# Optimization experiments

Measured on AMD Instinct MI355X. Metric: run time of the kernel, lower is better.

The kernel has to match this reference:

```python
import jax, jax.numpy as jnp
import numpy as np

N = 100000
IN_C = 128
OUT_C = 128
E = 1600000


def setup_inputs() -> dict:
    key = jax.random.key(0)
    k1, k2, k3, k4 = jax.random.split(key, 4)
    x = jax.random.normal(k1, (N, IN_C), dtype=jnp.float32)
    edge_index = jax.random.randint(k2, (2, E), 0, N, dtype=jnp.int64)
    # GCNConv params: linear weight (stored [in, out] for x @ W) and bias [out]
    W = jax.random.normal(k3, (IN_C, OUT_C), dtype=jnp.float32) / np.sqrt(IN_C)
    b = jax.random.normal(k4, (OUT_C,), dtype=jnp.float32) * 0.01
    return {"x": x, "edge_index": edge_index, "W": W, "b": b}


def reference(x, edge_index, W, b):
    n = x.shape[0]
    # add self loops (PyG GCNConv default add_self_loops=True)
    loop = jnp.arange(n, dtype=edge_index.dtype)
    src = jnp.concatenate([edge_index[0], loop])  # message sources
    dst = jnp.concatenate([edge_index[1], loop])  # aggregation targets
    # symmetric normalization: deg over targets (edge weight 1, incl. self loops)
    deg = jax.ops.segment_sum(jnp.ones_like(dst, dtype=x.dtype), dst, num_segments=n)
    dinv = jnp.where(deg > 0, jax.lax.rsqrt(deg), 0.0)
    norm = dinv[src] * dinv[dst]  # [E+N]
    # linear transform then gather-scale-scatter aggregation
    h = x @ W  # [N, out]
    msgs = h[src] * norm[:, None]  # [E+N, out] -- dominant memory traffic
    out = jax.ops.segment_sum(msgs, dst, num_segments=n)
    return out + b
```

## Files before the change

kernel.cpp:

```cpp
#include <hip/hip_runtime.h>


#define SCAN_T 256
#define SCAN_E 1024
#define WPB 4
#define CAP 1536
#define SC_T 8192

typedef __attribute__((ext_vector_type(8))) short short8;
typedef __attribute__((ext_vector_type(4))) float f32x4;

__device__ __forceinline__ unsigned short f2bf(float f) {
  unsigned int u = __float_as_uint(f);
  u += 0x7FFFu + ((u >> 16) & 1u);
  return (unsigned short)(u >> 16);
}
__device__ __forceinline__ float bf_lo(unsigned int u) { return __uint_as_float(u << 16); }
__device__ __forceinline__ float bf_hi(unsigned int u) { return __uint_as_float(u & 0xFFFF0000u); }


__global__ void k_zero(int* __restrict__ p, int m) {
  int i = blockIdx.x * blockDim.x + threadIdx.x;
  if (i < m) p[i] = 0;
}

__global__ void __launch_bounds__(512) k_scatter(
    const int* __restrict__ ei, int* __restrict__ bcursor,
    int* __restrict__ pairs, int E, int B) {
  __shared__ int hist[2048];
  int t = threadIdx.x;
  for (int b = t; b < B; b += 512) hist[b] = 0;
  __syncthreads();
  int e0 = blockIdx.x * SC_T;
  int eend = min(e0 + SC_T, E);
  for (int e = e0 + t * 4; e < eend; e += 2048) {
    if (e + 3 < eend) {
      int4 d = *(const int4*)(ei + E + e);
      atomicAdd(&hist[((unsigned)d.x) >> 6], 1);
      atomicAdd(&hist[((unsigned)d.y) >> 6], 1);
      atomicAdd(&hist[((unsigned)d.z) >> 6], 1);
      atomicAdd(&hist[((unsigned)d.w) >> 6], 1);
    } else {
      for (int q = e; q < eend; ++q) atomicAdd(&hist[((unsigned)ei[E + q]) >> 6], 1);
    }
  }
  __syncthreads();
  for (int b = t; b < B; b += 512) {
    int c = hist[b];
    hist[b] = c ? atomicAdd(&bcursor[b], c) : 0;
  }
  __syncthreads();
  for (int e = e0 + t * 4; e < eend; e += 2048) {
    if (e + 3 < eend) {
      int4 s = *(const int4*)(ei + e);
      int4 d = *(const int4*)(ei + E + e);
      int b0 = ((unsigned)d.x) >> 6; int p0 = atomicAdd(&hist[b0], 1);
      if (p0 < CAP) pairs[(size_t)b0 * CAP + p0] = ((d.x & 63) << 17) | s.x;
      int b1 = ((unsigned)d.y) >> 6; int p1 = atomicAdd(&hist[b1], 1);
      if (p1 < CAP) pairs[(size_t)b1 * CAP + p1] = ((d.y & 63) << 17) | s.y;
      int b2 = ((unsigned)d.z) >> 6; int p2 = atomicAdd(&hist[b2], 1);
      if (p2 < CAP) pairs[(size_t)b2 * CAP + p2] = ((d.z & 63) << 17) | s.z;
      int b3 = ((unsigned)d.w) >> 6; int p3 = atomicAdd(&hist[b3], 1);
      if (p3 < CAP) pairs[(size_t)b3 * CAP + p3] = ((d.w & 63) << 17) | s.w;
    } else {
      for (int q = e; q < eend; ++q) {
        int dst = ei[E + q], src = ei[q];
        int b0 = ((unsigned)dst) >> 6; int p0 = atomicAdd(&hist[b0], 1);
        if (p0 < CAP) pairs[(size_t)b0 * CAP + p0] = ((dst & 63) << 17) | src;
      }
    }
  }
}

__global__ void __launch_bounds__(256) k_sort_gemm(
    int* __restrict__ pairs, const int* __restrict__ bcursor,
    int* __restrict__ onc, float* __restrict__ dinv,
    const float* __restrict__ x, const float* __restrict__ W,
    unsigned short* __restrict__ h, int n) {
  __shared__ alignas(16) unsigned short Wt[128][136];
  __shared__ int pb[CAP];
  __shared__ int sorted[CAP];
  __shared__ int hist[64], base_[64], cur[64];
  __shared__ float dloc[64];
  int t = threadIdx.x;
  int b = blockIdx.x;
  if (t < 64) { hist[t] = 0; cur[t] = 0; }
  int cnt = min(bcursor[b], CAP);
  int* gp = pairs + (size_t)b * CAP;
  for (int i = t; i < cnt; i += 256) pb[i] = gp[i];
#pragma unroll
  for (int p = 0; p < 16; ++p) {
    int task = p * 256 + t;
    int kg = task >> 7, nn = task & 127;
    float w0 = W[(kg * 4 + 0) * 128 + nn];
    float w1 = W[(kg * 4 + 1) * 128 + nn];
    float w2 = W[(kg * 4 + 2) * 128 + nn];
    float w3 = W[(kg * 4 + 3) * 128 + nn];
    ushort4 u;
    u.x = f2bf(w0); u.y = f2bf(w1); u.z = f2bf(w2); u.w = f2bf(w3);
    *(ushort4*)&Wt[nn][kg * 4] = u;
  }
  __syncthreads();
  for (int i = t; i < cnt; i += 256) atomicAdd(&hist[pb[i] >> 17], 1);
  __syncthreads();
  if (t < 64) {
    int v = hist[t];
    int incl = v;
#pragma unroll
    for (int d = 1; d < 64; d <<= 1) {
      int u = __shfl_up(incl, d, 64);
      if (t >= d) incl += u;
    }
    base_[t] = incl - v;
    float di = rsqrtf((float)v + 1.0f);
    dloc[t] = di;
    int node = b * 64 + t;
    if (node < n) {
      onc[node] = ((incl - v) << 16) | v;
      dinv[node] = di;
    }
  }
  __syncthreads();
  for (int i = t; i < cnt; i += 256) {
    int p = pb[i];
    int d = p >> 17;
    int pos = base_[d] + atomicAdd(&cur[d], 1);
    sorted[pos] = p & 0x1FFFF;
  }
  __syncthreads();
  for (int i = t; i < cnt; i += 256) gp[i] = sorted[i];

  int w = t >> 6, lane = t & 63;
  int q = lane >> 4, m = lane & 15;
  int r0 = b * 64 + w * 16;
  f32x4 acc[8];
#pragma unroll
  for (int nt = 0; nt < 8; ++nt) acc[nt] = (f32x4){0.f, 0.f, 0.f, 0.f};
  float dscale[4];
#pragma unroll
  for (int rg = 0; rg < 4; ++rg) dscale[rg] = dloc[w * 16 + q * 4 + rg];
#pragma unroll
  for (int ks = 0; ks < 4; ++ks) {
    int row = r0 + m;
    row = row < n ? row : n - 1;
    const float* xp = x + (size_t)row * 128 + ks * 32 + q * 8;
    float4 a0 = *(const float4*)xp;
    float4 a1 = *(const float4*)(xp + 4);
    short8 af;
    af[0] = (short)f2bf(a0.x); af[1] = (short)f2bf(a0.y);
    af[2] = (short)f2bf(a0.z); af[3] = (short)f2bf(a0.w);
    af[4] = (short)f2bf(a1.x); af[5] = (short)f2bf(a1.y);
    af[6] = (short)f2bf(a1.z); af[7] = (short)f2bf(a1.w);
#pragma unroll
    for (int nt = 0; nt < 8; ++nt) {
      short8 bf = *(const short8*)&Wt[nt * 16 + m][ks * 32 + q * 8];
      acc[nt] = __builtin_amdgcn_mfma_f32_16x16x32_bf16(af, bf, acc[nt], 0, 0, 0);
    }
  }
#pragma unroll
  for (int nt = 0; nt < 8; ++nt)
#pragma unroll
    for (int rg = 0; rg < 4; ++rg) {
      int r = r0 + q * 4 + rg;
      if (r < n) h[(size_t)r * 128 + nt * 16 + m] = f2bf(acc[nt][rg] * dscale[rg]);
    }
}

__global__ void __launch_bounds__(256) k_agg_bias(
    const uint4* __restrict__ h4, const float* __restrict__ dinv,
    const int* __restrict__ onc, const int* __restrict__ pairs,
    const float* __restrict__ bias, float* __restrict__ out, int n) {
  int t = threadIdx.x;
  int lane = t & 63;
  int ln = lane & 15;
  int node = blockIdx.x * 16 + (t >> 6) * 4 + (lane >> 4);
  bool act = node < n;
  int nd = act ? node : n - 1;

  uint4 sp = h4[(size_t)nd * 16 + ln];
  float a[8];
  a[0] = bf_lo(sp.x); a[1] = bf_hi(sp.x);
  a[2] = bf_lo(sp.y); a[3] = bf_hi(sp.y);
  a[4] = bf_lo(sp.z); a[5] = bf_hi(sp.z);
  a[6] = bf_lo(sp.w); a[7] = bf_hi(sp.w);

  int v = act ? onc[nd] : 0;
  const int* __restrict__ csr = pairs + (size_t)(nd >> 6) * CAP + (v >> 16);
  int cnt = act ? (v & 0xFFFF) : 0;
  int s = 0;
  for (; s + 8 <= cnt; s += 8) {
    uint4 u[8];
#pragma unroll
    for (int k = 0; k < 8; ++k) {
      int idx = csr[s + k];
      u[k] = h4[(size_t)idx * 16 + ln];
    }
#pragma unroll
    for (int k = 0; k < 8; ++k) {
      a[0] += bf_lo(u[k].x); a[1] += bf_hi(u[k].x);
      a[2] += bf_lo(u[k].y); a[3] += bf_hi(u[k].y);
      a[4] += bf_lo(u[k].z); a[5] += bf_hi(u[k].z);
      a[6] += bf_lo(u[k].w); a[7] += bf_hi(u[k].w);
    }
  }
  for (; s + 4 <= cnt; s += 4) {
    uint4 u[4];
#pragma unroll
    for (int k = 0; k < 4; ++k) {
      int idx = csr[s + k];
      u[k] = h4[(size_t)idx * 16 + ln];
    }
#pragma unroll
    for (int k = 0; k < 4; ++k) {
      a[0] += bf_lo(u[k].x); a[1] += bf_hi(u[k].x);
      a[2] += bf_lo(u[k].y); a[3] += bf_hi(u[k].y);
      a[4] += bf_lo(u[k].z); a[5] += bf_hi(u[k].z);
      a[6] += bf_lo(u[k].w); a[7] += bf_hi(u[k].w);
    }
  }
  for (; s < cnt; ++s) {
    int idx = csr[s];
    uint4 u = h4[(size_t)idx * 16 + ln];
    a[0] += bf_lo(u.x); a[1] += bf_hi(u.x);
    a[2] += bf_lo(u.y); a[3] += bf_hi(u.y);
    a[4] += bf_lo(u.z); a[5] += bf_hi(u.z);
    a[6] += bf_lo(u.w); a[7] += bf_hi(u.w);
  }

  float di = dinv[nd];
  float4 b0 = ((const float4*)bias)[2 * ln];
  float4 b1 = ((const float4*)bias)[2 * ln + 1];
  f32x4 r0, r1;
  r0[0] = fmaf(a[0], di, b0.x); r0[1] = fmaf(a[1], di, b0.y);
  r0[2] = fmaf(a[2], di, b0.z); r0[3] = fmaf(a[3], di, b0.w);
  r1[0] = fmaf(a[4], di, b1.x); r1[1] = fmaf(a[5], di, b1.y);
  r1[2] = fmaf(a[6], di, b1.z); r1[3] = fmaf(a[7], di, b1.w);
  if (act) {
    f32x4* op = (f32x4*)(out + (size_t)nd * 128 + ln * 8);
    __builtin_nontemporal_store(r0, op);
    __builtin_nontemporal_store(r1, op + 1);
  }
}


__global__ void k_init(int* __restrict__ cnt, int n) {
  int i = blockIdx.x * blockDim.x + threadIdx.x;
  if (i < n) cnt[i] = 0;
}

__global__ void k_count4(const int* __restrict__ ei, int* __restrict__ cnt, int E) {
  int i = blockIdx.x * blockDim.x + threadIdx.x;
  int e = i * 4;
  if (e + 3 < E) {
    int4 d = *(const int4*)(ei + E + e);
    atomicAdd(&cnt[d.x], 1); atomicAdd(&cnt[d.y], 1);
    atomicAdd(&cnt[d.z], 1); atomicAdd(&cnt[d.w], 1);
  } else {
    for (; e < E; ++e) atomicAdd(&cnt[ei[E + e]], 1);
  }
}

__global__ void k_scan_local(const int* __restrict__ cnt, int* __restrict__ offs,
                             int* __restrict__ bsums, int n) {
  __shared__ int sh[SCAN_T];
  int t = threadIdx.x;
  int base = blockIdx.x * SCAN_E + t * 4;
  int v0 = 0, v1 = 0, v2 = 0, v3 = 0;
  if (base + 0 < n) v0 = cnt[base + 0];
  if (base + 1 < n) v1 = cnt[base + 1];
  if (base + 2 < n) v2 = cnt[base + 2];
  if (base + 3 < n) v3 = cnt[base + 3];
  int sum = v0 + v1 + v2 + v3;
  sh[t] = sum;
  __syncthreads();
  for (int d = 1; d < SCAN_T; d <<= 1) {
    int xv = (t >= d) ? sh[t - d] : 0;
    __syncthreads();
    sh[t] += xv;
    __syncthreads();
  }
  int run = sh[t] - sum;
  if (base + 0 < n) offs[base + 0] = run; run += v0;
  if (base + 1 < n) offs[base + 1] = run; run += v1;
  if (base + 2 < n) offs[base + 2] = run; run += v2;
  if (base + 3 < n) offs[base + 3] = run;
  if (t == SCAN_T - 1) bsums[blockIdx.x] = sh[t];
}

__global__ void k_scan_bsums(int* __restrict__ bsums, int nb) {
  __shared__ int sh[SCAN_T];
  int t = threadIdx.x;
  int v = (t < nb) ? bsums[t] : 0;
  sh[t] = v;
  __syncthreads();
  for (int d = 1; d < SCAN_T; d <<= 1) {
    int xv = (t >= d) ? sh[t - d] : 0;
    __syncthreads();
    sh[t] += xv;
    __syncthreads();
  }
  if (t < nb) bsums[t] = sh[t] - v;
}

__global__ void k_scan_finish(int* __restrict__ offs, const int* __restrict__ bsums,
                              const int* __restrict__ cnt, int* __restrict__ offs2,
                              float* __restrict__ dinv, int n) {
  int i = blockIdx.x * blockDim.x + threadIdx.x;
  if (i < n) {
    int o = offs[i] + bsums[i / SCAN_E];
    offs[i] = o;
    offs2[i] = o;
    dinv[i] = rsqrtf((float)cnt[i] + 1.0f);
  }
}

__global__ void k_fill4(const int* __restrict__ ei, int* __restrict__ offs2,
                        int* __restrict__ csr, int E) {
  int i = blockIdx.x * blockDim.x + threadIdx.x;
  int e = i * 4;
  if (e + 3 < E) {
    int4 s = *(const int4*)(ei + e);
    int4 d = *(const int4*)(ei + E + e);
    csr[atomicAdd(&offs2[d.x], 1)] = s.x;
    csr[atomicAdd(&offs2[d.y], 1)] = s.y;
    csr[atomicAdd(&offs2[d.z], 1)] = s.z;
    csr[atomicAdd(&offs2[d.w], 1)] = s.w;
  } else {
    for (; e < E; ++e) csr[atomicAdd(&offs2[ei[E + e]], 1)] = ei[e];
  }
}

__global__ void __launch_bounds__(256) k_gemm_h(
    const float* __restrict__ x, const float* __restrict__ W,
    const float* __restrict__ dinv, unsigned short* __restrict__ h, int n) {
  __shared__ alignas(16) unsigned short Wt[128][136];
  int t = threadIdx.x;
#pragma unroll
  for (int p = 0; p < 16; ++p) {
    int task = p * 256 + t;
    int kg = task >> 7, nn = task & 127;
    float w0 = W[(kg * 4 + 0) * 128 + nn];
    float w1 = W[(kg * 4 + 1) * 128 + nn];
    float w2 = W[(kg * 4 + 2) * 128 + nn];
    float w3 = W[(kg * 4 + 3) * 128 + nn];
    ushort4 u;
    u.x = f2bf(w0); u.y = f2bf(w1); u.z = f2bf(w2); u.w = f2bf(w3);
    *(ushort4*)&Wt[nn][kg * 4] = u;
  }
  __syncthreads();
  int w = t >> 6, lane = t & 63;
  int q = lane >> 4, m = lane & 15;
  int r0 = blockIdx.x * 64 + w * 16;
  f32x4 acc[8];
#pragma unroll
  for (int nt = 0; nt < 8; ++nt) acc[nt] = (f32x4){0.f, 0.f, 0.f, 0.f};
  float dscale[4];
#pragma unroll
  for (int rg = 0; rg < 4; ++rg) {
    int r = r0 + q * 4 + rg;
    dscale[rg] = dinv[r < n ? r : n - 1];
  }
#pragma unroll
  for (int ks = 0; ks < 4; ++ks) {
    int row = r0 + m;
    row = row < n ? row : n - 1;
    const float* xp = x + (size_t)row * 128 + ks * 32 + q * 8;
    float4 a0 = *(const float4*)xp;
    float4 a1 = *(const float4*)(xp + 4);
    short8 af;
    af[0] = (short)f2bf(a0.x); af[1] = (short)f2bf(a0.y);
    af[2] = (short)f2bf(a0.z); af[3] = (short)f2bf(a0.w);
    af[4] = (short)f2bf(a1.x); af[5] = (short)f2bf(a1.y);
    af[6] = (short)f2bf(a1.z); af[7] = (short)f2bf(a1.w);
#pragma unroll
    for (int nt = 0; nt < 8; ++nt) {
      short8 bf = *(const short8*)&Wt[nt * 16 + m][ks * 32 + q * 8];
      acc[nt] = __builtin_amdgcn_mfma_f32_16x16x32_bf16(af, bf, acc[nt], 0, 0, 0);
    }
  }
#pragma unroll
  for (int nt = 0; nt < 8; ++nt)
#pragma unroll
    for (int rg = 0; rg < 4; ++rg) {
      int r = r0 + q * 4 + rg;
      if (r < n) h[(size_t)r * 128 + nt * 16 + m] = f2bf(acc[nt][rg] * dscale[rg]);
    }
}

__global__ void __launch_bounds__(256) k_agg_bias_csr(
    const unsigned int* __restrict__ h2, const float* __restrict__ dinv,
    const int* __restrict__ offs, const int* __restrict__ cnt,
    const int* __restrict__ csr, const float* __restrict__ bias,
    float* __restrict__ out, int n) {
  int node = blockIdx.x * WPB + (threadIdx.x >> 6);
  int lane = threadIdx.x & 63;
  if (node >= n) return;
  unsigned int sp = h2[(size_t)node * 64 + lane];
  float ax = bf_lo(sp), ay = bf_hi(sp);
  int s = offs[node];
  int end = s + cnt[node];
  for (; s + 8 <= end; s += 8) {
    int i0 = csr[s + 0], i1 = csr[s + 1], i2 = csr[s + 2], i3 = csr[s + 3];
    int i4 = csr[s + 4], i5 = csr[s + 5], i6 = csr[s + 6], i7 = csr[s + 7];
    unsigned int u0 = h2[(size_t)i0 * 64 + lane];
    unsigned int u1 = h2[(size_t)i1 * 64 + lane];
    unsigned int u2 = h2[(size_t)i2 * 64 + lane];
    unsigned int u3 = h2[(size_t)i3 * 64 + lane];
    unsigned int u4 = h2[(size_t)i4 * 64 + lane];
    unsigned int u5 = h2[(size_t)i5 * 64 + lane];
    unsigned int u6 = h2[(size_t)i6 * 64 + lane];
    unsigned int u7 = h2[(size_t)i7 * 64 + lane];
    ax += (bf_lo(u0) + bf_lo(u1)) + (bf_lo(u2) + bf_lo(u3)) +
          (bf_lo(u4) + bf_lo(u5)) + (bf_lo(u6) + bf_lo(u7));
    ay += (bf_hi(u0) + bf_hi(u1)) + (bf_hi(u2) + bf_hi(u3)) +
          (bf_hi(u4) + bf_hi(u5)) + (bf_hi(u6) + bf_hi(u7));
  }
  for (; s < end; ++s) {
    unsigned int u = h2[(size_t)csr[s] * 64 + lane];
    ax += bf_lo(u); ay += bf_hi(u);
  }
  float di = dinv[node];
  float2 bb = ((const float2*)bias)[lane];
  float2 r;
  r.x = fmaf(ax, di, bb.x);
  r.y = fmaf(ay, di, bb.y);
  ((float2*)out)[(size_t)node * 64 + lane] = r;
}

extern "C" void kernel_launch(void* const* d_in, const int* in_sizes, int n_in,
                              void* d_out, int out_size, void* d_ws, size_t ws_size,
                              hipStream_t stream) {
  const float* x = (const float*)d_in[0];
  const int* ei = (const int*)d_in[1];
  const float* Wm = (const float*)d_in[2];
  const float* bias = (const float*)d_in[3];
  float* out = (float*)d_out;

  int N = in_sizes[0] / 128;
  int E = in_sizes[1] / 2;
  int NB = (N + 63) >> 6;

  size_t need_new = (size_t)N * 8 + 8192 + (size_t)NB * CAP * 4 + (size_t)N * 256;

  if (ws_size >= need_new && N <= (1 << 17) && NB <= 2048) {
    char* p = (char*)d_ws;
    float* dinv = (float*)p;       p += (size_t)N * 4;
    int* onc = (int*)p;            p += (size_t)N * 4;
    int* bcursor = (int*)p;        p += 8192;
    int* pairs = (int*)p;          p += (size_t)NB * CAP * 4;
    unsigned short* h = (unsigned short*)p;

    k_zero<<<(NB + 255) / 256, 256, 0, stream>>>(bcursor, NB);
    k_scatter<<<(E + SC_T - 1) / SC_T, 512, 0, stream>>>(ei, bcursor, pairs, E, NB);
    k_sort_gemm<<<NB, 256, 0, stream>>>(pairs, bcursor, onc, dinv, x, Wm, h, N);
    k_agg_bias<<<(N + 15) / 16, 256, 0, stream>>>(
        (const uint4*)h, dinv, onc, pairs, bias, out, N);
    return;
  }

  char* p = (char*)d_ws;
  int* cnt = (int*)p;        p += (size_t)N * 4;
  int* offs = (int*)p;       p += (size_t)N * 4;
  int* offs2 = (int*)p;      p += (size_t)N * 4;
  float* dinv = (float*)p;   p += (size_t)N * 4;
  int* bsums = (int*)p;      p += 1024;
  int* csr = (int*)p;        p += (size_t)E * 4;
  unsigned short* h = (unsigned short*)p;

  int nb_n = (N + 255) / 256;
  int nb_e4 = ((E + 3) / 4 + 255) / 256;
  int nb_scan = (N + SCAN_E - 1) / SCAN_E;

  k_init<<<nb_n, 256, 0, stream>>>(cnt, N);
  k_count4<<<nb_e4, 256, 0, stream>>>(ei, cnt, E);
  k_scan_local<<<nb_scan, SCAN_T, 0, stream>>>(cnt, offs, bsums, N);
  k_scan_bsums<<<1, SCAN_T, 0, stream>>>(bsums, nb_scan);
  k_scan_finish<<<nb_n, 256, 0, stream>>>(offs, bsums, cnt, offs2, dinv, N);
  k_fill4<<<nb_e4, 256, 0, stream>>>(ei, offs2, csr, E);
  k_gemm_h<<<(N + 63) / 64, 256, 0, stream>>>(x, Wm, dinv, h, N);
  k_agg_bias_csr<<<(N + WPB - 1) / WPB, 256, 0, stream>>>(
      (const unsigned int*)h, dinv, offs, cnt, csr, bias, out, N);
}
```

Before: 208.2 us.

## Move bucket sort into aggregation kernel and compute degrees via global atomics

Node degrees are now counted with global atomics during the scatter pass, so the GEMM kernel no longer sorts bucket pairs. It reads the degree array directly to scale h. The per-bucket counting sort moves into the aggregation kernel, which keeps the sorted CSR in shared memory and aggregates the bucket's 64 nodes from it. This removes the global write-back and re-read of the sorted pairs and the onc/dinv arrays. In exchange it adds 1.6M global atomics in the scatter kernel and gives the aggregation kernel fewer, larger blocks that hold more shared memory.

New measurement: 259.5 us. +24.6%, slower.

```diff
diff --git a/kernel.cpp b/kernel.cpp
--- a/kernel.cpp
+++ b/kernel.cpp
@@ -25,7 +25,7 @@
 }
 
 __global__ void __launch_bounds__(512) k_scatter(
-    const int* __restrict__ ei, int* __restrict__ bcursor,
+    const int* __restrict__ ei, int* __restrict__ deg, int* __restrict__ bcursor,
     int* __restrict__ pairs, int E, int B) {
   __shared__ int hist[2048];
   int t = threadIdx.x;
@@ -40,8 +40,16 @@
       atomicAdd(&hist[((unsigned)d.y) >> 6], 1);
       atomicAdd(&hist[((unsigned)d.z) >> 6], 1);
       atomicAdd(&hist[((unsigned)d.w) >> 6], 1);
+      atomicAdd(&deg[d.x], 1);
+      atomicAdd(&deg[d.y], 1);
+      atomicAdd(&deg[d.z], 1);
+      atomicAdd(&deg[d.w], 1);
     } else {
-      for (int q = e; q < eend; ++q) atomicAdd(&hist[((unsigned)ei[E + q]) >> 6], 1);
+      for (int q = e; q < eend; ++q) {
+        int dst = ei[E + q];
+        atomicAdd(&hist[((unsigned)dst) >> 6], 1);
+        atomicAdd(&deg[dst], 1);
+      }
     }
   }
   __syncthreads();
@@ -72,22 +80,11 @@
   }
 }
 
-__global__ void __launch_bounds__(256) k_sort_gemm(
-    int* __restrict__ pairs, const int* __restrict__ bcursor,
-    int* __restrict__ onc, float* __restrict__ dinv,
+__global__ void __launch_bounds__(256) k_gemm_h2(
     const float* __restrict__ x, const float* __restrict__ W,
-    unsigned short* __restrict__ h, int n) {
+    const int* __restrict__ cnt, unsigned short* __restrict__ h, int n) {
   __shared__ alignas(16) unsigned short Wt[128][136];
-  __shared__ int pb[CAP];
-  __shared__ int sorted[CAP];
-  __shared__ int hist[64], base_[64], cur[64];
-  __shared__ float dloc[64];
-  int t = threadIdx.x;
-  int b = blockIdx.x;
-  if (t < 64) { hist[t] = 0; cur[t] = 0; }
-  int cnt = min(bcursor[b], CAP);
-  int* gp = pairs + (size_t)b * CAP;
-  for (int i = t; i < cnt; i += 256) pb[i] = gp[i];
+  int t = threadIdx.x;
 #pragma unroll
   for (int p = 0; p < 16; ++p) {
     int task = p * 256 + t;
@@ -101,44 +98,18 @@
     *(ushort4*)&Wt[nn][kg * 4] = u;
   }
   __syncthreads();
-  for (int i = t; i < cnt; i += 256) atomicAdd(&hist[pb[i] >> 17], 1);
-  __syncthreads();
-  if (t < 64) {
-    int v = hist[t];
-    int incl = v;
-#pragma unroll
-    for (int d = 1; d < 64; d <<= 1) {
-      int u = __shfl_up(incl, d, 64);
-      if (t >= d) incl += u;
-    }
-    base_[t] = incl - v;
-    float di = rsqrtf((float)v + 1.0f);
-    dloc[t] = di;
-    int node = b * 64 + t;
-    if (node < n) {
-      onc[node] = ((incl - v) << 16) | v;
-      dinv[node] = di;
-    }
-  }
-  __syncthreads();
-  for (int i = t; i < cnt; i += 256) {
-    int p = pb[i];
-    int d = p >> 17;
-    int pos = base_[d] + atomicAdd(&cur[d], 1);
-    sorted[pos] = p & 0x1FFFF;
-  }
-  __syncthreads();
-  for (int i = t; i < cnt; i += 256) gp[i] = sorted[i];
-
   int w = t >> 6, lane = t & 63;
   int q = lane >> 4, m = lane & 15;
-  int r0 = b * 64 + w * 16;
+  int r0 = blockIdx.x * 64 + w * 16;
   f32x4 acc[8];
 #pragma unroll
   for (int nt = 0; nt < 8; ++nt) acc[nt] = (f32x4){0.f, 0.f, 0.f, 0.f};
   float dscale[4];
 #pragma unroll
-  for (int rg = 0; rg < 4; ++rg) dscale[rg] = dloc[w * 16 + q * 4 + rg];
+  for (int rg = 0; rg < 4; ++rg) {
+    int r = r0 + q * 4 + rg;
+    dscale[rg] = rsqrtf((float)cnt[r < n ? r : n - 1] + 1.0f);
+  }
 #pragma unroll
   for (int ks = 0; ks < 4; ++ks) {
     int row = r0 + m;
@@ -166,79 +137,112 @@
     }
 }
 
-__global__ void __launch_bounds__(256) k_agg_bias(
-    const uint4* __restrict__ h4, const float* __restrict__ dinv,
-    const int* __restrict__ onc, const int* __restrict__ pairs,
-    const float* __restrict__ bias, float* __restrict__ out, int n) {
-  int t = threadIdx.x;
-  int lane = t & 63;
-  int ln = lane & 15;
-  int node = blockIdx.x * 16 + (t >> 6) * 4 + (lane >> 4);
-  bool act = node < n;
-  int nd = act ? node : n - 1;
-
-  uint4 sp = h4[(size_t)nd * 16 + ln];
-  float a[8];
-  a[0] = bf_lo(sp.x); a[1] = bf_hi(sp.x);
-  a[2] = bf_lo(sp.y); a[3] = bf_hi(sp.y);
-  a[4] = bf_lo(sp.z); a[5] = bf_hi(sp.z);
-  a[6] = bf_lo(sp.w); a[7] = bf_hi(sp.w);
-
-  int v = act ? onc[nd] : 0;
-  const int* __restrict__ csr = pairs + (size_t)(nd >> 6) * CAP + (v >> 16);
-  int cnt = act ? (v & 0xFFFF) : 0;
-  int s = 0;
-  for (; s + 8 <= cnt; s += 8) {
-    uint4 u[8];
-#pragma unroll
-    for (int k = 0; k < 8; ++k) {
-      int idx = csr[s + k];
-      u[k] = h4[(size_t)idx * 16 + ln];
-    }
-#pragma unroll
-    for (int k = 0; k < 8; ++k) {
-      a[0] += bf_lo(u[k].x); a[1] += bf_hi(u[k].x);
-      a[2] += bf_lo(u[k].y); a[3] += bf_hi(u[k].y);
-      a[4] += bf_lo(u[k].z); a[5] += bf_hi(u[k].z);
-      a[6] += bf_lo(u[k].w); a[7] += bf_hi(u[k].w);
-    }
-  }
-  for (; s + 4 <= cnt; s += 4) {
-    uint4 u[4];
-#pragma unroll
-    for (int k = 0; k < 4; ++k) {
-      int idx = csr[s + k];
-      u[k] = h4[(size_t)idx * 16 + ln];
-    }
-#pragma unroll
-    for (int k = 0; k < 4; ++k) {
-      a[0] += bf_lo(u[k].x); a[1] += bf_hi(u[k].x);
-      a[2] += bf_lo(u[k].y); a[3] += bf_hi(u[k].y);
-      a[4] += bf_lo(u[k].z); a[5] += bf_hi(u[k].z);
-      a[6] += bf_lo(u[k].w); a[7] += bf_hi(u[k].w);
-    }
-  }
-  for (; s < cnt; ++s) {
-    int idx = csr[s];
-    uint4 u = h4[(size_t)idx * 16 + ln];
-    a[0] += bf_lo(u.x); a[1] += bf_hi(u.x);
-    a[2] += bf_lo(u.y); a[3] += bf_hi(u.y);
-    a[4] += bf_lo(u.z); a[5] += bf_hi(u.z);
-    a[6] += bf_lo(u.w); a[7] += bf_hi(u.w);
-  }
-
-  float di = dinv[nd];
-  float4 b0 = ((const float4*)bias)[2 * ln];
-  float4 b1 = ((const float4*)bias)[2 * ln + 1];
-  f32x4 r0, r1;
-  r0[0] = fmaf(a[0], di, b0.x); r0[1] = fmaf(a[1], di, b0.y);
-  r0[2] = fmaf(a[2], di, b0.z); r0[3] = fmaf(a[3], di, b0.w);
-  r1[0] = fmaf(a[4], di, b1.x); r1[1] = fmaf(a[5], di, b1.y);
-  r1[2] = fmaf(a[6], di, b1.z); r1[3] = fmaf(a[7], di, b1.w);
-  if (act) {
-    f32x4* op = (f32x4*)(out + (size_t)nd * 128 + ln * 8);
-    __builtin_nontemporal_store(r0, op);
-    __builtin_nontemporal_store(r1, op + 1);
+__global__ void __launch_bounds__(256) k_sort_agg(
+    const int* __restrict__ pairs, const int* __restrict__ bcursor,
+    const uint4* __restrict__ h4, const float* __restrict__ bias,
+    float* __restrict__ out, int n) {
+  __shared__ int pb[CAP];
+  __shared__ int sorted[CAP];
+  __shared__ int hist[64], base_[64], cur[64];
+  int t = threadIdx.x;
+  int b = blockIdx.x;
+  if (t < 64) { hist[t] = 0; cur[t] = 0; }
+  __syncthreads();
+  int cnt = min(bcursor[b], CAP);
+  const int* __restrict__ gp = pairs + (size_t)b * CAP;
+  for (int i = t; i < cnt; i += 256) {
+    int p = gp[i];
+    pb[i] = p;
+    atomicAdd(&hist[p >> 17], 1);
+  }
+  __syncthreads();
+  if (t < 64) {
+    int v = hist[t];
+    int incl = v;
+#pragma unroll
+    for (int d = 1; d < 64; d <<= 1) {
+      int u = __shfl_up(incl, d, 64);
+      if (t >= d) incl += u;
+    }
+    base_[t] = incl - v;
+  }
+  __syncthreads();
+  for (int i = t; i < cnt; i += 256) {
+    int p = pb[i];
+    int d = p >> 17;
+    int pos = base_[d] + atomicAdd(&cur[d], 1);
+    sorted[pos] = p & 0x1FFFF;
+  }
+  __syncthreads();
+
+  int g = t >> 4, ln = t & 15;
+  int nbase = b << 6;
+#pragma unroll
+  for (int rep = 0; rep < 4; ++rep) {
+    int row = g + rep * 16;
+    int node = nbase + row;
+    bool act = node < n;
+    uint4 sp = make_uint4(0u, 0u, 0u, 0u);
+    if (act) sp = h4[(size_t)node * 16 + ln];
+    float a[8];
+    a[0] = bf_lo(sp.x); a[1] = bf_hi(sp.x);
+    a[2] = bf_lo(sp.y); a[3] = bf_hi(sp.y);
+    a[4] = bf_lo(sp.z); a[5] = bf_hi(sp.z);
+    a[6] = bf_lo(sp.w); a[7] = bf_hi(sp.w);
+    int s = base_[row];
+    int cd = hist[row];
+    int end = s + cd;
+    for (; s + 8 <= end; s += 8) {
+      uint4 u[8];
+#pragma unroll
+      for (int k = 0; k < 8; ++k) {
+        int idx = sorted[s + k];
+        u[k] = h4[(size_t)idx * 16 + ln];
+      }
+#pragma unroll
+      for (int k = 0; k < 8; ++k) {
+        a[0] += bf_lo(u[k].x); a[1] += bf_hi(u[k].x);
+        a[2] += bf_lo(u[k].y); a[3] += bf_hi(u[k].y);
+        a[4] += bf_lo(u[k].z); a[5] += bf_hi(u[k].z);
+        a[6] += bf_lo(u[k].w); a[7] += bf_hi(u[k].w);
+      }
+    }
+    for (; s + 4 <= end; s += 4) {
+      uint4 u[4];
+#pragma unroll
+      for (int k = 0; k < 4; ++k) {
+        int idx = sorted[s + k];
+        u[k] = h4[(size_t)idx * 16 + ln];
+      }
+#pragma unroll
+      for (int k = 0; k < 4; ++k) {
+        a[0] += bf_lo(u[k].x); a[1] += bf_hi(u[k].x);
+        a[2] += bf_lo(u[k].y); a[3] += bf_hi(u[k].y);
+        a[4] += bf_lo(u[k].z); a[5] += bf_hi(u[k].z);
+        a[6] += bf_lo(u[k].w); a[7] += bf_hi(u[k].w);
+      }
+    }
+    for (; s < end; ++s) {
+      int idx = sorted[s];
+      uint4 u = h4[(size_t)idx * 16 + ln];
+      a[0] += bf_lo(u.x); a[1] += bf_hi(u.x);
+      a[2] += bf_lo(u.y); a[3] += bf_hi(u.y);
+      a[4] += bf_lo(u.z); a[5] += bf_hi(u.z);
+      a[6] += bf_lo(u.w); a[7] += bf_hi(u.w);
+    }
+    if (act) {
+      float di = rsqrtf((float)cd + 1.0f);
+      float4 b0 = ((const float4*)bias)[2 * ln];
+      float4 b1 = ((const float4*)bias)[2 * ln + 1];
+      f32x4 r0, r1;
+      r0[0] = fmaf(a[0], di, b0.x); r0[1] = fmaf(a[1], di, b0.y);
+      r0[2] = fmaf(a[2], di, b0.z); r0[3] = fmaf(a[3], di, b0.w);
+      r1[0] = fmaf(a[4], di, b1.x); r1[1] = fmaf(a[5], di, b1.y);
+      r1[2] = fmaf(a[6], di, b1.z); r1[3] = fmaf(a[7], di, b1.w);
+      f32x4* op = (f32x4*)(out + (size_t)node * 128 + ln * 8);
+      __builtin_nontemporal_store(r0, op);
+      __builtin_nontemporal_store(r1, op + 1);
+    }
   }
 }
 
@@ -440,21 +444,26 @@
   int E = in_sizes[1] / 2;
   int NB = (N + 63) >> 6;
 
-  size_t need_new = (size_t)N * 8 + 8192 + (size_t)NB * CAP * 4 + (size_t)N * 256;
-
-  if (ws_size >= need_new && N <= (1 << 17) && NB <= 2048) {
+  int nb_n = (N + 255) / 256;
+  int nb_e4 = ((E + 3) / 4 + 255) / 256;
+
+  size_t off_bc = ((size_t)N * 4 + 255) & ~(size_t)255;
+  size_t off_pairs = off_bc + 8192;
+  size_t off_h = (off_pairs + (size_t)NB * CAP * 4 + 255) & ~(size_t)255;
+  size_t need11 = off_h + (size_t)N * 256;
+
+  if (ws_size >= need11 && N <= (1 << 17) && NB <= 2048) {
     char* p = (char*)d_ws;
-    float* dinv = (float*)p;       p += (size_t)N * 4;
-    int* onc = (int*)p;            p += (size_t)N * 4;
-    int* bcursor = (int*)p;        p += 8192;
-    int* pairs = (int*)p;          p += (size_t)NB * CAP * 4;
-    unsigned short* h = (unsigned short*)p;
-
-    k_zero<<<(NB + 255) / 256, 256, 0, stream>>>(bcursor, NB);
-    k_scatter<<<(E + SC_T - 1) / SC_T, 512, 0, stream>>>(ei, bcursor, pairs, E, NB);
-    k_sort_gemm<<<NB, 256, 0, stream>>>(pairs, bcursor, onc, dinv, x, Wm, h, N);
-    k_agg_bias<<<(N + 15) / 16, 256, 0, stream>>>(
-        (const uint4*)h, dinv, onc, pairs, bias, out, N);
+    int* deg = (int*)p;
+    int* bcursor = (int*)(p + off_bc);
+    int* pairs = (int*)(p + off_pairs);
+    unsigned short* h = (unsigned short*)(p + off_h);
+
+    int zcnt = (int)(off_pairs / 4);
+    k_zero<<<(zcnt + 255) / 256, 256, 0, stream>>>((int*)p, zcnt);
+    k_scatter<<<(E + SC_T - 1) / SC_T, 512, 0, stream>>>(ei, deg, bcursor, pairs, E, NB);
+    k_gemm_h2<<<NB, 256, 0, stream>>>(x, Wm, deg, h, N);
+    k_sort_agg<<<NB, 256, 0, stream>>>(pairs, bcursor, (const uint4*)h, bias, out, N);
     return;
   }
 
@@ -467,8 +476,6 @@
   int* csr = (int*)p;        p += (size_t)E * 4;
   unsigned short* h = (unsigned short*)p;
 
-  int nb_n = (N + 255) / 256;
-  int nb_e4 = ((E + 3) / 4 + 255) / 256;
   int nb_scan = (N + SCAN_E - 1) / SCAN_E;
 
   k_init<<<nb_n, 256, 0, stream>>>(cnt, N);
```
